# Optimization experiments

Hardware: AMD Instinct MI355X
Metric: run time of the kernel (lower is better)

The kernel has to match this reference:

```python
import jax, jax.numpy as jnp
import numpy as np

HIDDEN = 512
HEADS = 8
HEAD_DIM = HIDDEN // HEADS


def setup_inputs() -> dict:
    key = jax.random.key(0)
    ks = jax.random.split(key, 13)
    B, S, H = 4, 2048, HIDDEN
    s = 1.0 / np.sqrt(H).astype(np.float32)
    inp = {
        "values": jax.random.normal(ks[0], (B, S, H), jnp.float32),
        "keys": jax.random.normal(ks[1], (B, S, H), jnp.float32),
        "query": jax.random.normal(ks[2], (B, S, H), jnp.float32),
        "mask": jax.random.randint(ks[3], (B, S), 0, 2, jnp.int32),
        "Wq": jax.random.normal(ks[4], (H, H), jnp.float32) * s,
        "bq": jnp.zeros((H,), jnp.float32),
        "Wk": jax.random.normal(ks[5], (H, H), jnp.float32) * s,
        "bk": jnp.zeros((H,), jnp.float32),
        "Wv": jax.random.normal(ks[6], (H, H), jnp.float32) * s,
        "bv": jnp.zeros((H,), jnp.float32),
        "Wo": jax.random.normal(ks[7], (H, H), jnp.float32) * s,
        "bo": jnp.zeros((H,), jnp.float32),
    }
    return inp


def reference(values, keys, query, mask, Wq, bq, Wk, bk, Wv, bv, Wo, bo):
    B, Sq, H = query.shape
    Sk = keys.shape[1]
    # projections (x @ W + b)
    Q = query @ Wq + bq
    K = keys @ Wk + bk
    V = values @ Wv + bv
    # [B, S, H] -> [B, heads, S, head_dim]
    def split(x, S):
        return x.reshape(B, S, HEADS, HEAD_DIM).transpose(0, 2, 1, 3)
    Qh, Kh, Vh = split(Q, Sq), split(K, Sk), split(V, Sk)
    scale = 1.0 / np.sqrt(HEAD_DIM).astype(np.float32)
    scores = jnp.einsum('bhqd,bhkd->bhqk', Qh, Kh) * scale  # [B,H,Sq,Sk]
    m = mask[:, None, None, :]  # [B,1,1,Sk]
    scores = jnp.where(m == 0, jnp.float32(-1e9), scores)
    attn = jax.nn.softmax(scores, axis=-1)
    ctx = jnp.einsum('bhqk,bhkd->bhqd', attn, Vh)
    ctx = ctx.transpose(0, 2, 1, 3).reshape(B, Sq, H)
    return ctx @ Wo + bo
```

## Files before the change

### kernel.cpp

```cpp
#include <hip/hip_runtime.h>

#define HID 512
#define NH 8
#define HD 64
#define BATCH 4
#define SEQ 2048
#define MTOT (BATCH * SEQ)

typedef unsigned short ushort_t;
typedef __bf16 bf16x8 __attribute__((ext_vector_type(8)));
typedef unsigned short ushort8v __attribute__((ext_vector_type(8)));
typedef unsigned short ushort4v __attribute__((ext_vector_type(4)));
typedef float floatx4 __attribute__((ext_vector_type(4)));

static __device__ __forceinline__ unsigned short f2bf(float f) {
  __bf16 b = (__bf16)f;
  return __builtin_bit_cast(unsigned short, b);
}
static __device__ __forceinline__ float bf2f(unsigned short s) {
  union { unsigned int u; float f; } c; c.u = ((unsigned int)s) << 16;
  return c.f;
}
static __device__ __forceinline__ bf16x8 asbf(ushort8v v) {
  return __builtin_bit_cast(bf16x8, v);
}
static __device__ __forceinline__ float max3f(float a, float b, float c) {
  return fmaxf(fmaxf(a, b), c);
}

#define SC_LOG2E 0.18033688011112042f

__global__ void detect_dtype(const unsigned int* __restrict__ q, int* __restrict__ flag) {
  if (threadIdx.x == 0 && blockIdx.x == 0) {
    int hits = 0;
    for (int i = 0; i < 256; ++i) {
      unsigned e = (q[i] >> 7) & 0xff;
      hits += (e >= 110 && e <= 136) ? 1 : 0;
    }
    flag[0] = (hits >= 128) ? 1 : 0;
  }
}

__global__ __launch_bounds__(256) void prep_w(
    const void* __restrict__ W0, const void* __restrict__ W1,
    const void* __restrict__ W2, const void* __restrict__ W3,
    ushort_t* __restrict__ T0, ushort_t* __restrict__ T1,
    ushort_t* __restrict__ T2, ushort_t* __restrict__ T3,
    const int* __restrict__ flag) {
  const int isbf = flag[0];
  const void* W; ushort_t* T;
  switch (blockIdx.y) {
    case 0: W = W0; T = T0; break;
    case 1: W = W1; T = T1; break;
    case 2: W = W2; T = T2; break;
    default: W = W3; T = T3; break;
  }
  int idx = blockIdx.x * 256 + threadIdx.x;
  int k = idx >> 9, n = idx & 511;
  ushort_t v = isbf ? ((const ushort_t*)W)[k * HID + n]
                    : f2bf(((const float*)W)[k * HID + n]);
  T[n * HID + k] = v;
}

__global__ __launch_bounds__(256) void prep_b(
    const void* __restrict__ B0, const void* __restrict__ B1,
    const void* __restrict__ B2, const void* __restrict__ B3,
    float* __restrict__ biasF, const int* __restrict__ flag) {
  const int isbf = flag[0];
  int i = blockIdx.x * 256 + threadIdx.x;
  int t = i >> 9, j = i & 511;
  const void* B = (t == 0) ? B0 : (t == 1) ? B1 : (t == 2) ? B2 : B3;
  biasF[i] = isbf ? bf2f(((const ushort_t*)B)[j]) : ((const float*)B)[j];
}

__global__ __launch_bounds__(256) void prep_mask(
    const int* __restrict__ mask, float* __restrict__ mb) {
  int i = blockIdx.x * 256 + threadIdx.x;
  mb[i] = mask[i] ? 0.f : -1e9f;
}

__global__ __launch_bounds__(256) void gemm_qkv(
    const void* __restrict__ X0, const void* __restrict__ X1, const void* __restrict__ X2,
    const ushort_t* __restrict__ WtBase, const float* __restrict__ biasBase,
    ushort_t* __restrict__ YBase, const int* __restrict__ flag) {
  const int isbf = flag[0];
  const int z = blockIdx.z;
  const void* X = (z == 0) ? X0 : (z == 1) ? X1 : X2;
  const ushort_t* Wt = WtBase + (size_t)z * HID * HID;
  const float* biasF = biasBase + (size_t)z * HID;
  ushort_t* Y = YBase + (size_t)z * MTOT * HID;

  const int tid = threadIdx.x;
  const int wid = tid >> 6, lane = tid & 63;
  const int id = lane & 15, quad = lane >> 4;
  const int wm = wid >> 1, wn = wid & 1;
  const int m0 = blockIdx.x * 64, n0 = blockIdx.y * 128;

  __shared__ ushort_t At[64 * 72];
  __shared__ ushort_t Bt[128 * 72];

  const int srow = tid >> 3;
  const int scol = (tid & 7) * 8;

  floatx4 acc[2][4];
#pragma unroll
  for (int i = 0; i < 2; ++i)
#pragma unroll
    for (int j = 0; j < 4; ++j) acc[i][j] = (floatx4){0.f, 0.f, 0.f, 0.f};

  for (int k0 = 0; k0 < HID; k0 += 64) {
    ushort8v aR[2], bR[4];
    if (isbf) {
      const ushort_t* ap = (const ushort_t*)X + (long)(m0 + srow) * HID + k0 + scol;
#pragma unroll
      for (int p = 0; p < 2; ++p) aR[p] = *(const ushort8v*)(ap + (long)p * 32 * HID);
    } else {
      const float* apf = (const float*)X + (long)(m0 + srow) * HID + k0 + scol;
#pragma unroll
      for (int p = 0; p < 2; ++p) {
        floatx4 f0 = *(const floatx4*)(apf + (long)p * 32 * HID);
        floatx4 f1 = *(const floatx4*)(apf + (long)p * 32 * HID + 4);
#pragma unroll
        for (int i = 0; i < 4; ++i) { aR[p][i] = f2bf(f0[i]); aR[p][4 + i] = f2bf(f1[i]); }
      }
    }
    {
      const ushort_t* bp = Wt + (long)(n0 + srow) * HID + k0 + scol;
#pragma unroll
      for (int p = 0; p < 4; ++p) bR[p] = *(const ushort8v*)(bp + (long)p * 32 * HID);
    }
    __syncthreads();
#pragma unroll
    for (int p = 0; p < 2; ++p) *(ushort8v*)(&At[(srow + 32 * p) * 72 + scol]) = aR[p];
#pragma unroll
    for (int p = 0; p < 4; ++p) *(ushort8v*)(&Bt[(srow + 32 * p) * 72 + scol]) = bR[p];
    __syncthreads();
#pragma unroll
    for (int kk = 0; kk < 64; kk += 32) {
      ushort8v af[2], bf4[4];
#pragma unroll
      for (int ms = 0; ms < 2; ++ms) af[ms] = *(const ushort8v*)(&At[(wm * 32 + ms * 16 + id) * 72 + kk + quad * 8]);
#pragma unroll
      for (int ns = 0; ns < 4; ++ns) bf4[ns] = *(const ushort8v*)(&Bt[(wn * 64 + ns * 16 + id) * 72 + kk + quad * 8]);
#pragma unroll
      for (int ms = 0; ms < 2; ++ms)
#pragma unroll
        for (int ns = 0; ns < 4; ++ns)
          acc[ms][ns] = __builtin_amdgcn_mfma_f32_16x16x32_bf16(asbf(af[ms]), asbf(bf4[ns]), acc[ms][ns], 0, 0, 0);
    }
  }
#pragma unroll
  for (int ns = 0; ns < 4; ++ns) {
    float bv = biasF[n0 + wn * 64 + ns * 16 + id];
    int col = n0 + wn * 64 + ns * 16 + id;
#pragma unroll
    for (int ms = 0; ms < 2; ++ms) {
      int row0 = m0 + wm * 32 + ms * 16 + quad * 4;
#pragma unroll
      for (int r = 0; r < 4; ++r)
        Y[(long)(row0 + r) * HID + col] = f2bf(acc[ms][ns][r] + bv);
    }
  }
}

__global__ __launch_bounds__(256) void gemm_lds_out(
    const ushort_t* __restrict__ X, const ushort_t* __restrict__ Wt,
    const float* __restrict__ biasF, void* __restrict__ out,
    const int* __restrict__ flag) {
  const int isbf = flag[0];
  const int tid = threadIdx.x;
  const int wid = tid >> 6, lane = tid & 63;
  const int id = lane & 15, quad = lane >> 4;
  const int wm = wid >> 1, wn = wid & 1;
  const int m0 = blockIdx.x * 64, n0 = blockIdx.y * 128;

  __shared__ ushort_t At[64 * 72];
  __shared__ ushort_t Bt[128 * 72];

  const int srow = tid >> 3;
  const int scol = (tid & 7) * 8;

  floatx4 acc[2][4];
#pragma unroll
  for (int i = 0; i < 2; ++i)
#pragma unroll
    for (int j = 0; j < 4; ++j) acc[i][j] = (floatx4){0.f, 0.f, 0.f, 0.f};

  for (int k0 = 0; k0 < HID; k0 += 64) {
    ushort8v aR[2], bR[4];
    {
      const ushort_t* ap = X + (long)(m0 + srow) * HID + k0 + scol;
#pragma unroll
      for (int p = 0; p < 2; ++p) aR[p] = *(const ushort8v*)(ap + (long)p * 32 * HID);
      const ushort_t* bp = Wt + (long)(n0 + srow) * HID + k0 + scol;
#pragma unroll
      for (int p = 0; p < 4; ++p) bR[p] = *(const ushort8v*)(bp + (long)p * 32 * HID);
    }
    __syncthreads();
#pragma unroll
    for (int p = 0; p < 2; ++p) *(ushort8v*)(&At[(srow + 32 * p) * 72 + scol]) = aR[p];
#pragma unroll
    for (int p = 0; p < 4; ++p) *(ushort8v*)(&Bt[(srow + 32 * p) * 72 + scol]) = bR[p];
    __syncthreads();
#pragma unroll
    for (int kk = 0; kk < 64; kk += 32) {
      ushort8v af[2], bf4[4];
#pragma unroll
      for (int ms = 0; ms < 2; ++ms) af[ms] = *(const ushort8v*)(&At[(wm * 32 + ms * 16 + id) * 72 + kk + quad * 8]);
#pragma unroll
      for (int ns = 0; ns < 4; ++ns) bf4[ns] = *(const ushort8v*)(&Bt[(wn * 64 + ns * 16 + id) * 72 + kk + quad * 8]);
#pragma unroll
      for (int ms = 0; ms < 2; ++ms)
#pragma unroll
        for (int ns = 0; ns < 4; ++ns)
          acc[ms][ns] = __builtin_amdgcn_mfma_f32_16x16x32_bf16(asbf(af[ms]), asbf(bf4[ns]), acc[ms][ns], 0, 0, 0);
    }
  }
#pragma unroll
  for (int ns = 0; ns < 4; ++ns) {
    float bv = biasF[n0 + wn * 64 + ns * 16 + id];
    int col = n0 + wn * 64 + ns * 16 + id;
#pragma unroll
    for (int ms = 0; ms < 2; ++ms) {
      int row0 = m0 + wm * 32 + ms * 16 + quad * 4;
      if (isbf) {
        ushort_t* o = (ushort_t*)out;
#pragma unroll
        for (int r = 0; r < 4; ++r) o[(long)(row0 + r) * HID + col] = f2bf(acc[ms][ns][r] + bv);
      } else {
        float* o = (float*)out;
#pragma unroll
        for (int r = 0; r < 4; ++r) o[(long)(row0 + r) * HID + col] = acc[ms][ns][r] + bv;
      }
    }
  }
}

__global__ __launch_bounds__(256) void flash_attn(
    const ushort_t* __restrict__ Q, const ushort_t* __restrict__ K,
    const ushort_t* __restrict__ V, const float* __restrict__ mb,
    ushort_t* __restrict__ ctx) {
  const int qblk = blockIdx.x, h = blockIdx.y, b = blockIdx.z;
  const int tid = threadIdx.x;
  const int wid = tid >> 6, lane = tid & 63;
  const int id = lane & 15, quad = lane >> 4;

  __shared__ ushort_t Kt[64 * 72];
  __shared__ ushort_t Vt[64 * 72];
  __shared__ ushort_t Pl[4][32 * 72];

  const ushort_t* Qb = Q + (long)(b * SEQ + qblk * 128 + wid * 32) * HID + h * HD;
  const ushort_t* Kb = K + (long)(b * SEQ) * HID + h * HD;
  const ushort_t* Vb = V + (long)(b * SEQ) * HID + h * HD;
  const float* mrow = mb + b * SEQ;

  ushort8v qf[2][2];
#pragma unroll
  for (int qs = 0; qs < 2; ++qs)
#pragma unroll
    for (int kh = 0; kh < 2; ++kh)
      qf[qs][kh] = *(const ushort8v*)(Qb + (qs * 16 + id) * HID + kh * 32 + quad * 8);

  floatx4 o[4][2];
  float m_i[2] = {-1e30f, -1e30f}, l_i[2] = {0.f, 0.f};
#pragma unroll
  for (int dg = 0; dg < 4; ++dg) { o[dg][0] = (floatx4){0,0,0,0}; o[dg][1] = (floatx4){0,0,0,0}; }

  const int skey = tid >> 2;
  const int sdc  = (tid & 3) * 16;
  const int vkp  = (tid & 31) * 2;
  const int vdc  = (tid >> 5) * 8;

  ushort8v k0v, k1v, v0v, v1v;
  {
    const ushort_t* kpp = Kb + (long)skey * HID + sdc;
    k0v = *(const ushort8v*)(kpp);
    k1v = *(const ushort8v*)(kpp + 8);
    const ushort_t* vp0 = Vb + (long)vkp * HID + vdc;
    v0v = *(const ushort8v*)(vp0);
    v1v = *(const ushort8v*)(vp0 + HID);
  }

  for (int kb = 0; kb < SEQ / 64; ++kb) {
    *(ushort8v*)(&Kt[skey * 72 + sdc])     = k0v;
    *(ushort8v*)(&Kt[skey * 72 + sdc + 8]) = k1v;
#pragma unroll
    for (int i = 0; i < 8; ++i) {
      unsigned int dw = (unsigned int)v0v[i] | ((unsigned int)v1v[i] << 16);
      *(unsigned int*)(&Vt[(vdc + i) * 72 + vkp]) = dw;
    }
    __syncthreads();

    if (kb + 1 < SEQ / 64) {
      const ushort_t* kpp = Kb + (long)((kb + 1) * 64 + skey) * HID + sdc;
      k0v = *(const ushort8v*)(kpp);
      k1v = *(const ushort8v*)(kpp + 8);
      const ushort_t* vp0 = Vb + (long)((kb + 1) * 64 + vkp) * HID + vdc;
      v0v = *(const ushort8v*)(vp0);
      v1v = *(const ushort8v*)(vp0 + HID);
    }

    floatx4 st[2][4];
#pragma unroll
    for (int ks = 0; ks < 4; ++ks) {
      ushort8v kf0 = *(const ushort8v*)(&Kt[(ks * 16 + id) * 72 + quad * 8]);
      ushort8v kf1 = *(const ushort8v*)(&Kt[(ks * 16 + id) * 72 + 32 + quad * 8]);
#pragma unroll
      for (int qs = 0; qs < 2; ++qs) {
        floatx4 a = (floatx4){0,0,0,0};
        a = __builtin_amdgcn_mfma_f32_16x16x32_bf16(asbf(kf0), asbf(qf[qs][0]), a, 0, 0, 0);
        a = __builtin_amdgcn_mfma_f32_16x16x32_bf16(asbf(kf1), asbf(qf[qs][1]), a, 0, 0, 0);
        st[qs][ks] = a;
      }
    }
#pragma unroll
    for (int ks = 0; ks < 4; ++ks) {
      floatx4 mbv = *(const floatx4*)(mrow + kb * 64 + ks * 16 + quad * 4);
#pragma unroll
      for (int r = 0; r < 4; ++r) {
        st[0][ks][r] = fmaf(st[0][ks][r], SC_LOG2E, mbv[r]);
        st[1][ks][r] = fmaf(st[1][ks][r], SC_LOG2E, mbv[r]);
      }
    }
#pragma unroll
    for (int qs = 0; qs < 2; ++qs) {
      float a0 = max3f(st[qs][0][0], st[qs][0][1], st[qs][0][2]);
      float a1 = max3f(st[qs][0][3], st[qs][1][0], st[qs][1][1]);
      float a2 = max3f(st[qs][1][2], st[qs][1][3], st[qs][2][0]);
      float a3 = max3f(st[qs][2][1], st[qs][2][2], st[qs][2][3]);
      float a4 = max3f(st[qs][3][0], st[qs][3][1], st[qs][3][2]);
      float mx = max3f(a0, a1, st[qs][3][3]);
      float mz = max3f(a2, a3, a4);
      mx = fmaxf(mx, mz);
      mx = fmaxf(mx, __shfl_xor(mx, 16));
      mx = fmaxf(mx, __shfl_xor(mx, 32));
      if (!__all(mx - m_i[qs] <= 8.f)) {
        float mnew = fmaxf(m_i[qs], mx);
        float alpha = exp2f(m_i[qs] - mnew);
        m_i[qs] = mnew;
        l_i[qs] *= alpha;
#pragma unroll
        for (int dg = 0; dg < 4; ++dg) o[dg][qs] *= alpha;
      }
      float mcur = m_i[qs];
      float rs = 0.f;
#pragma unroll
      for (int ks = 0; ks < 4; ++ks) {
        ushort4v pk;
#pragma unroll
        for (int r = 0; r < 4; ++r) {
          float p = exp2f(st[qs][ks][r] - mcur);
          rs += p;
          pk[r] = f2bf(p);
        }
        *(ushort4v*)(&Pl[wid][(qs * 16 + id) * 72 + ks * 16 + quad * 4]) = pk;
      }
      rs += __shfl_xor(rs, 16);
      rs += __shfl_xor(rs, 32);
      l_i[qs] += rs;
    }

#pragma unroll
    for (int kc = 0; kc < 2; ++kc) {
      ushort8v pf0 = *(const ushort8v*)(&Pl[wid][(0 * 16 + id) * 72 + kc * 32 + quad * 8]);
      ushort8v pf1 = *(const ushort8v*)(&Pl[wid][(1 * 16 + id) * 72 + kc * 32 + quad * 8]);
#pragma unroll
      for (int dg = 0; dg < 4; ++dg) {
        ushort8v vf = *(const ushort8v*)(&Vt[(dg * 16 + id) * 72 + kc * 32 + quad * 8]);
        o[dg][0] = __builtin_amdgcn_mfma_f32_16x16x32_bf16(asbf(vf), asbf(pf0), o[dg][0], 0, 0, 0);
        o[dg][1] = __builtin_amdgcn_mfma_f32_16x16x32_bf16(asbf(vf), asbf(pf1), o[dg][1], 0, 0, 0);
      }
    }
    __syncthreads();
  }

#pragma unroll
  for (int qs = 0; qs < 2; ++qs) {
    float inv = 1.0f / l_i[qs];
    long qrow = (long)(b * SEQ + qblk * 128 + wid * 32 + qs * 16 + id);
#pragma unroll
    for (int dg = 0; dg < 4; ++dg) {
      ushort4v pk;
#pragma unroll
      for (int r = 0; r < 4; ++r) pk[r] = f2bf(o[dg][qs][r] * inv);
      *(ushort4v*)(&ctx[qrow * HID + h * HD + dg * 16 + quad * 4]) = pk;
    }
  }
}

extern "C" void kernel_launch(void* const* d_in, const int* in_sizes, int n_in,
                              void* d_out, int out_size, void* d_ws, size_t ws_size,
                              hipStream_t stream) {
  const void* values = d_in[0];
  const void* keys   = d_in[1];
  const void* query  = d_in[2];
  const int*  mask   = (const int*)d_in[3];
  const void* Wq = d_in[4];  const void* bq = d_in[5];
  const void* Wk = d_in[6];  const void* bk = d_in[7];
  const void* Wv = d_in[8];  const void* bv = d_in[9];
  const void* Wo = d_in[10]; const void* bo = d_in[11];

  ushort_t* ws = (ushort_t*)d_ws;
  const size_t NEL = (size_t)MTOT * HID;
  ushort_t* Qp  = ws;
  ushort_t* Kp  = ws + NEL;
  ushort_t* Vp  = ws + 2 * NEL;
  ushort_t* Cp  = ws + 3 * NEL;
  ushort_t* WqT = ws + 4 * NEL;
  ushort_t* WkT = WqT + (size_t)HID * HID;
  ushort_t* WvT = WkT + (size_t)HID * HID;
  ushort_t* WoT = WvT + (size_t)HID * HID;
  float* biasF  = (float*)(WoT + (size_t)HID * HID);
  float* mbias  = biasF + 4 * HID;
  int* flag     = (int*)(mbias + (size_t)BATCH * SEQ);

  detect_dtype<<<1, 64, 0, stream>>>((const unsigned int*)query, flag);
  prep_w<<<dim3(1024, 4), 256, 0, stream>>>(Wq, Wk, Wv, Wo, WqT, WkT, WvT, WoT, flag);
  prep_b<<<8, 256, 0, stream>>>(bq, bk, bv, bo, biasF, flag);
  prep_mask<<<MTOT / 256, 256, 0, stream>>>(mask, mbias);

  gemm_qkv<<<dim3(MTOT / 64, HID / 128, 3), 256, 0, stream>>>(
      query, keys, values, WqT, biasF, Qp, flag);

  flash_attn<<<dim3(SEQ / 128, NH, BATCH), 256, 0, stream>>>(Qp, Kp, Vp, mbias, Cp);

  gemm_lds_out<<<dim3(MTOT / 64, HID / 128), 256, 0, stream>>>(
      Cp, WoT, biasF + 3 * HID, d_out, flag);
}
```

Baseline: 240.5 us.

## Use direct global-to-LDS loads with XOR swizzle and pre-convert inputs to bf16

Adds a prep_x kernel that converts the fp32 query/keys/values to bf16 in workspace. Both GEMMs now stage tiles through global_load_lds with an XOR-swizzled LDS layout instead of register staging with padding, and the QKV GEMM tile grows to 128x128. In flash attention, the V transpose uses byte-perm instructions, exp2 calls the hardware intrinsic, and the row sum is split into four partial accumulators. The extra conversion pass adds a full read and write of the inputs, in exchange for cheaper GEMM loads.

```diff
diff --git a/kernel.cpp b/kernel.cpp
--- a/kernel.cpp
+++ b/kernel.cpp
@@ -12,6 +12,7 @@
 typedef unsigned short ushort8v __attribute__((ext_vector_type(8)));
 typedef unsigned short ushort4v __attribute__((ext_vector_type(4)));
 typedef float floatx4 __attribute__((ext_vector_type(4)));
+typedef unsigned int uintx4 __attribute__((ext_vector_type(4)));
 
 static __device__ __forceinline__ unsigned short f2bf(float f) {
   __bf16 b = (__bf16)f;
@@ -26,6 +27,14 @@
 }
 static __device__ __forceinline__ float max3f(float a, float b, float c) {
   return fmaxf(fmaxf(a, b), c);
+}
+static __device__ __forceinline__ float fexp2(float x) {
+  return __builtin_amdgcn_exp2f(x);
+}
+static __device__ __forceinline__ void gl_lds16(const ushort_t* g, ushort_t* l) {
+  __builtin_amdgcn_global_load_lds(
+      (const __attribute__((address_space(1))) void*)g,
+      (__attribute__((address_space(3))) void*)l, 16, 0, 0);
 }
 
 #define SC_LOG2E 0.18033688011112042f
@@ -79,13 +88,31 @@
   mb[i] = mask[i] ? 0.f : -1e9f;
 }
 
-__global__ __launch_bounds__(256) void gemm_qkv(
-    const void* __restrict__ X0, const void* __restrict__ X1, const void* __restrict__ X2,
-    const ushort_t* __restrict__ WtBase, const float* __restrict__ biasBase,
-    ushort_t* __restrict__ YBase, const int* __restrict__ flag) {
+__global__ __launch_bounds__(256) void prep_x(
+    const void* __restrict__ X0, const void* __restrict__ X1,
+    const void* __restrict__ X2, ushort_t* __restrict__ Xb,
+    const int* __restrict__ flag) {
   const int isbf = flag[0];
+  const int z = blockIdx.y;
+  const void* X = (z == 0) ? X0 : (z == 1) ? X1 : X2;
+  long i = (long)(blockIdx.x * 256 + threadIdx.x) * 8;
+  ushort8v o;
+  if (isbf) {
+    o = *(const ushort8v*)((const ushort_t*)X + i);
+  } else {
+    floatx4 f0 = *(const floatx4*)((const float*)X + i);
+    floatx4 f1 = *(const floatx4*)((const float*)X + i + 4);
+#pragma unroll
+    for (int r = 0; r < 4; ++r) { o[r] = f2bf(f0[r]); o[4 + r] = f2bf(f1[r]); }
+  }
+  *(ushort8v*)(Xb + (size_t)z * MTOT * HID + i) = o;
+}
+
+__global__ __launch_bounds__(256) void gemm_qkv2(
+    const ushort_t* __restrict__ Xb, const ushort_t* __restrict__ WtBase,
+    const float* __restrict__ biasBase, ushort_t* __restrict__ YBase) {
   const int z = blockIdx.z;
-  const void* X = (z == 0) ? X0 : (z == 1) ? X1 : X2;
+  const ushort_t* X = Xb + (size_t)z * MTOT * HID;
   const ushort_t* Wt = WtBase + (size_t)z * HID * HID;
   const float* biasF = biasBase + (size_t)z * HID;
   ushort_t* Y = YBase + (size_t)z * MTOT * HID;
@@ -94,68 +121,61 @@
   const int wid = tid >> 6, lane = tid & 63;
   const int id = lane & 15, quad = lane >> 4;
   const int wm = wid >> 1, wn = wid & 1;
-  const int m0 = blockIdx.x * 64, n0 = blockIdx.y * 128;
-
-  __shared__ ushort_t At[64 * 72];
-  __shared__ ushort_t Bt[128 * 72];
-
-  const int srow = tid >> 3;
-  const int scol = (tid & 7) * 8;
-
-  floatx4 acc[2][4];
-#pragma unroll
-  for (int i = 0; i < 2; ++i)
+  const int m0 = blockIdx.x * 128, n0 = blockIdx.y * 128;
+
+  __shared__ ushort_t As[128 * 64];
+  __shared__ ushort_t Bs[128 * 64];
+
+  const int lrow = lane >> 3;
+  const int scb  = (lane & 7) ^ lrow;
+
+  floatx4 acc[4][4];
+#pragma unroll
+  for (int i = 0; i < 4; ++i)
 #pragma unroll
     for (int j = 0; j < 4; ++j) acc[i][j] = (floatx4){0.f, 0.f, 0.f, 0.f};
 
   for (int k0 = 0; k0 < HID; k0 += 64) {
-    ushort8v aR[2], bR[4];
-    if (isbf) {
-      const ushort_t* ap = (const ushort_t*)X + (long)(m0 + srow) * HID + k0 + scol;
-#pragma unroll
-      for (int p = 0; p < 2; ++p) aR[p] = *(const ushort8v*)(ap + (long)p * 32 * HID);
-    } else {
-      const float* apf = (const float*)X + (long)(m0 + srow) * HID + k0 + scol;
-#pragma unroll
-      for (int p = 0; p < 2; ++p) {
-        floatx4 f0 = *(const floatx4*)(apf + (long)p * 32 * HID);
-        floatx4 f1 = *(const floatx4*)(apf + (long)p * 32 * HID + 4);
-#pragma unroll
-        for (int i = 0; i < 4; ++i) { aR[p][i] = f2bf(f0[i]); aR[p][4 + i] = f2bf(f1[i]); }
-      }
-    }
-    {
-      const ushort_t* bp = Wt + (long)(n0 + srow) * HID + k0 + scol;
-#pragma unroll
-      for (int p = 0; p < 4; ++p) bR[p] = *(const ushort8v*)(bp + (long)p * 32 * HID);
-    }
-    __syncthreads();
-#pragma unroll
-    for (int p = 0; p < 2; ++p) *(ushort8v*)(&At[(srow + 32 * p) * 72 + scol]) = aR[p];
-#pragma unroll
-    for (int p = 0; p < 4; ++p) *(ushort8v*)(&Bt[(srow + 32 * p) * 72 + scol]) = bR[p];
+    __syncthreads();
+#pragma unroll
+    for (int i = 0; i < 4; ++i) {
+      int r = wid * 32 + i * 8 + lrow;
+      gl_lds16(X + (long)(m0 + r) * HID + k0 + scb * 8, &As[(wid * 32 + i * 8) * 64]);
+    }
+#pragma unroll
+    for (int i = 0; i < 4; ++i) {
+      int r = wid * 32 + i * 8 + lrow;
+      gl_lds16(Wt + (long)(n0 + r) * HID + k0 + scb * 8, &Bs[(wid * 32 + i * 8) * 64]);
+    }
     __syncthreads();
 #pragma unroll
     for (int kk = 0; kk < 64; kk += 32) {
-      ushort8v af[2], bf4[4];
-#pragma unroll
-      for (int ms = 0; ms < 2; ++ms) af[ms] = *(const ushort8v*)(&At[(wm * 32 + ms * 16 + id) * 72 + kk + quad * 8]);
-#pragma unroll
-      for (int ns = 0; ns < 4; ++ns) bf4[ns] = *(const ushort8v*)(&Bt[(wn * 64 + ns * 16 + id) * 72 + kk + quad * 8]);
-#pragma unroll
-      for (int ms = 0; ms < 2; ++ms)
+      ushort8v af[4], bfv[4];
+      const int cb = (kk >> 3) + quad;
+#pragma unroll
+      for (int ms = 0; ms < 4; ++ms) {
+        int row = wm * 64 + ms * 16 + id;
+        af[ms] = *(const ushort8v*)(&As[row * 64 + ((cb ^ (id & 7)) << 3)]);
+      }
+#pragma unroll
+      for (int ns = 0; ns < 4; ++ns) {
+        int row = wn * 64 + ns * 16 + id;
+        bfv[ns] = *(const ushort8v*)(&Bs[row * 64 + ((cb ^ (id & 7)) << 3)]);
+      }
+#pragma unroll
+      for (int ms = 0; ms < 4; ++ms)
 #pragma unroll
         for (int ns = 0; ns < 4; ++ns)
-          acc[ms][ns] = __builtin_amdgcn_mfma_f32_16x16x32_bf16(asbf(af[ms]), asbf(bf4[ns]), acc[ms][ns], 0, 0, 0);
+          acc[ms][ns] = __builtin_amdgcn_mfma_f32_16x16x32_bf16(asbf(af[ms]), asbf(bfv[ns]), acc[ms][ns], 0, 0, 0);
     }
   }
 #pragma unroll
   for (int ns = 0; ns < 4; ++ns) {
-    float bv = biasF[n0 + wn * 64 + ns * 16 + id];
     int col = n0 + wn * 64 + ns * 16 + id;
-#pragma unroll
-    for (int ms = 0; ms < 2; ++ms) {
-      int row0 = m0 + wm * 32 + ms * 16 + quad * 4;
+    float bv = biasF[col];
+#pragma unroll
+    for (int ms = 0; ms < 4; ++ms) {
+      int row0 = m0 + wm * 64 + ms * 16 + quad * 4;
 #pragma unroll
       for (int r = 0; r < 4; ++r)
         Y[(long)(row0 + r) * HID + col] = f2bf(acc[ms][ns][r] + bv);
@@ -163,7 +183,7 @@
   }
 }
 
-__global__ __launch_bounds__(256) void gemm_lds_out(
+__global__ __launch_bounds__(256) void gemm_out2(
     const ushort_t* __restrict__ X, const ushort_t* __restrict__ Wt,
     const float* __restrict__ biasF, void* __restrict__ out,
     const int* __restrict__ flag) {
@@ -174,11 +194,11 @@
   const int wm = wid >> 1, wn = wid & 1;
   const int m0 = blockIdx.x * 64, n0 = blockIdx.y * 128;
 
-  __shared__ ushort_t At[64 * 72];
-  __shared__ ushort_t Bt[128 * 72];
-
-  const int srow = tid >> 3;
-  const int scol = (tid & 7) * 8;
+  __shared__ ushort_t As[64 * 64];
+  __shared__ ushort_t Bs[128 * 64];
+
+  const int lrow = lane >> 3;
+  const int scb  = (lane & 7) ^ lrow;
 
   floatx4 acc[2][4];
 #pragma unroll
@@ -187,39 +207,43 @@
     for (int j = 0; j < 4; ++j) acc[i][j] = (floatx4){0.f, 0.f, 0.f, 0.f};
 
   for (int k0 = 0; k0 < HID; k0 += 64) {
-    ushort8v aR[2], bR[4];
-    {
-      const ushort_t* ap = X + (long)(m0 + srow) * HID + k0 + scol;
-#pragma unroll
-      for (int p = 0; p < 2; ++p) aR[p] = *(const ushort8v*)(ap + (long)p * 32 * HID);
-      const ushort_t* bp = Wt + (long)(n0 + srow) * HID + k0 + scol;
-#pragma unroll
-      for (int p = 0; p < 4; ++p) bR[p] = *(const ushort8v*)(bp + (long)p * 32 * HID);
-    }
-    __syncthreads();
-#pragma unroll
-    for (int p = 0; p < 2; ++p) *(ushort8v*)(&At[(srow + 32 * p) * 72 + scol]) = aR[p];
-#pragma unroll
-    for (int p = 0; p < 4; ++p) *(ushort8v*)(&Bt[(srow + 32 * p) * 72 + scol]) = bR[p];
+    __syncthreads();
+#pragma unroll
+    for (int i = 0; i < 2; ++i) {
+      int r = wid * 16 + i * 8 + lrow;
+      gl_lds16(X + (long)(m0 + r) * HID + k0 + scb * 8, &As[(wid * 16 + i * 8) * 64]);
+    }
+#pragma unroll
+    for (int i = 0; i < 4; ++i) {
+      int r = wid * 32 + i * 8 + lrow;
+      gl_lds16(Wt + (long)(n0 + r) * HID + k0 + scb * 8, &Bs[(wid * 32 + i * 8) * 64]);
+    }
     __syncthreads();
 #pragma unroll
     for (int kk = 0; kk < 64; kk += 32) {
-      ushort8v af[2], bf4[4];
-#pragma unroll
-      for (int ms = 0; ms < 2; ++ms) af[ms] = *(const ushort8v*)(&At[(wm * 32 + ms * 16 + id) * 72 + kk + quad * 8]);
-#pragma unroll
-      for (int ns = 0; ns < 4; ++ns) bf4[ns] = *(const ushort8v*)(&Bt[(wn * 64 + ns * 16 + id) * 72 + kk + quad * 8]);
+      ushort8v af[2], bfv[4];
+      const int cb = (kk >> 3) + quad;
+#pragma unroll
+      for (int ms = 0; ms < 2; ++ms) {
+        int row = wm * 32 + ms * 16 + id;
+        af[ms] = *(const ushort8v*)(&As[row * 64 + ((cb ^ (id & 7)) << 3)]);
+      }
+#pragma unroll
+      for (int ns = 0; ns < 4; ++ns) {
+        int row = wn * 64 + ns * 16 + id;
+        bfv[ns] = *(const ushort8v*)(&Bs[row * 64 + ((cb ^ (id & 7)) << 3)]);
+      }
 #pragma unroll
       for (int ms = 0; ms < 2; ++ms)
 #pragma unroll
         for (int ns = 0; ns < 4; ++ns)
-          acc[ms][ns] = __builtin_amdgcn_mfma_f32_16x16x32_bf16(asbf(af[ms]), asbf(bf4[ns]), acc[ms][ns], 0, 0, 0);
+          acc[ms][ns] = __builtin_amdgcn_mfma_f32_16x16x32_bf16(asbf(af[ms]), asbf(bfv[ns]), acc[ms][ns], 0, 0, 0);
     }
   }
 #pragma unroll
   for (int ns = 0; ns < 4; ++ns) {
-    float bv = biasF[n0 + wn * 64 + ns * 16 + id];
     int col = n0 + wn * 64 + ns * 16 + id;
+    float bv = biasF[col];
 #pragma unroll
     for (int ms = 0; ms < 2; ++ms) {
       int row0 = m0 + wm * 32 + ms * 16 + quad * 4;
@@ -284,10 +308,16 @@
   for (int kb = 0; kb < SEQ / 64; ++kb) {
     *(ushort8v*)(&Kt[skey * 72 + sdc])     = k0v;
     *(ushort8v*)(&Kt[skey * 72 + sdc + 8]) = k1v;
-#pragma unroll
-    for (int i = 0; i < 8; ++i) {
-      unsigned int dw = (unsigned int)v0v[i] | ((unsigned int)v1v[i] << 16);
-      *(unsigned int*)(&Vt[(vdc + i) * 72 + vkp]) = dw;
+    {
+      uintx4 a = __builtin_bit_cast(uintx4, v0v);
+      uintx4 bq = __builtin_bit_cast(uintx4, v1v);
+#pragma unroll
+      for (int j = 0; j < 4; ++j) {
+        unsigned int d0 = __builtin_amdgcn_perm(bq[j], a[j], 0x05040100u);
+        unsigned int d1 = __builtin_amdgcn_perm(bq[j], a[j], 0x07060302u);
+        *(unsigned int*)(&Vt[(vdc + 2 * j) * 72 + vkp])     = d0;
+        *(unsigned int*)(&Vt[(vdc + 2 * j + 1) * 72 + vkp]) = d1;
+      }
     }
     __syncthreads();
 
@@ -336,25 +366,26 @@
       mx = fmaxf(mx, __shfl_xor(mx, 32));
       if (!__all(mx - m_i[qs] <= 8.f)) {
         float mnew = fmaxf(m_i[qs], mx);
-        float alpha = exp2f(m_i[qs] - mnew);
+        float alpha = fexp2(m_i[qs] - mnew);
         m_i[qs] = mnew;
         l_i[qs] *= alpha;
 #pragma unroll
         for (int dg = 0; dg < 4; ++dg) o[dg][qs] *= alpha;
       }
       float mcur = m_i[qs];
-      float rs = 0.f;
+      floatx4 rsv = (floatx4){0.f, 0.f, 0.f, 0.f};
 #pragma unroll
       for (int ks = 0; ks < 4; ++ks) {
         ushort4v pk;
 #pragma unroll
         for (int r = 0; r < 4; ++r) {
-          float p = exp2f(st[qs][ks][r] - mcur);
-          rs += p;
+          float p = fexp2(st[qs][ks][r] - mcur);
+          rsv[r] += p;
           pk[r] = f2bf(p);
         }
         *(ushort4v*)(&Pl[wid][(qs * 16 + id) * 72 + ks * 16 + quad * 4]) = pk;
       }
+      float rs = (rsv[0] + rsv[1]) + (rsv[2] + rsv[3]);
       rs += __shfl_xor(rs, 16);
       rs += __shfl_xor(rs, 32);
       l_i[qs] += rs;
@@ -406,7 +437,8 @@
   ushort_t* Kp  = ws + NEL;
   ushort_t* Vp  = ws + 2 * NEL;
   ushort_t* Cp  = ws + 3 * NEL;
-  ushort_t* WqT = ws + 4 * NEL;
+  ushort_t* Xb  = ws + 4 * NEL;
+  ushort_t* WqT = ws + 7 * NEL;
   ushort_t* WkT = WqT + (size_t)HID * HID;
   ushort_t* WvT = WkT + (size_t)HID * HID;
   ushort_t* WoT = WvT + (size_t)HID * HID;
@@ -418,12 +450,12 @@
   prep_w<<<dim3(1024, 4), 256, 0, stream>>>(Wq, Wk, Wv, Wo, WqT, WkT, WvT, WoT, flag);
   prep_b<<<8, 256, 0, stream>>>(bq, bk, bv, bo, biasF, flag);
   prep_mask<<<MTOT / 256, 256, 0, stream>>>(mask, mbias);
-
-  gemm_qkv<<<dim3(MTOT / 64, HID / 128, 3), 256, 0, stream>>>(
-      query, keys, values, WqT, biasF, Qp, flag);
+  prep_x<<<dim3(MTOT * HID / (256 * 8), 3), 256, 0, stream>>>(query, keys, values, Xb, flag);
+
+  gemm_qkv2<<<dim3(MTOT / 128, HID / 128, 3), 256, 0, stream>>>(Xb, WqT, biasF, Qp);
 
   flash_attn<<<dim3(SEQ / 128, NH, BATCH), 256, 0, stream>>>(Qp, Kp, Vp, mbias, Cp);
 
-  gemm_lds_out<<<dim3(MTOT / 64, HID / 128), 256, 0, stream>>>(
+  gemm_out2<<<dim3(MTOT / 64, HID / 128), 256, 0, stream>>>(
       Cp, WoT, biasF + 3 * HID, d_out, flag);
 }
```

Result: faster. 231.3 us (-3.8%).
